# Kernel optimization log

Hardware: AMD Instinct MI355X
Metric: run time of the kernel (lower is better)

Reference implementation:

```python
import jax, jax.numpy as jnp
import numpy as np

N_NODES = 50000
N_EDGES = 800000
N_GRAPHS = 128
IN, HID, OUT, CLS = 128, 128, 128, 10


def setup_inputs() -> dict:
    key = jax.random.key(0)
    ks = jax.random.split(key, 16)
    d = {}
    d["features"] = jax.random.normal(ks[0], (N_NODES, IN), jnp.float32)
    d["edge_src"] = jax.random.randint(ks[1], (N_EDGES,), 0, N_NODES)
    d["edge_dst"] = jax.random.randint(ks[2], (N_EDGES,), 0, N_NODES)
    d["graph_ids"] = jnp.sort(jax.random.randint(ks[3], (N_NODES,), 0, N_GRAPHS))

    def lin(k, i, o):
        return (jax.random.normal(k, (i, o), jnp.float32) / np.float32(np.sqrt(i)))

    dims = [(IN, HID), (HID, HID), (HID, OUT)]
    for l, (i, o) in enumerate(dims):
        d[f"Ws{l}"] = lin(ks[4 + 3 * l], i, o)
        d[f"Wn{l}"] = lin(ks[5 + 3 * l], i, o)
        d[f"b{l}"] = jnp.zeros((o,), jnp.float32)
    d["Wf"] = lin(ks[13], OUT, CLS)
    d["bf"] = jnp.zeros((CLS,), jnp.float32)
    return d


def _sage_mean_layer(h, edge_src, edge_dst, Ws, Wn, b, in_deg):
    # mean-aggregate in-neighbor features: gather at src, segment-sum at dst
    msg_sum = jax.ops.segment_sum(h[edge_src], edge_dst, num_segments=N_NODES)
    h_neigh = msg_sum / in_deg  # [N, d], zero-degree nodes divide by 1 -> 0
    return jax.nn.relu(h @ Ws + h_neigh @ Wn + b)


def reference(features, edge_src, edge_dst, graph_ids,
              Ws0, Wn0, b0, Ws1, Wn1, b1, Ws2, Wn2, b2, Wf, bf):
    ones = jnp.ones((N_EDGES,), jnp.float32)
    in_deg = jax.ops.segment_sum(ones, edge_dst, num_segments=N_NODES)
    in_deg = jnp.maximum(in_deg, 1.0)[:, None]  # [N, 1]

    h = features
    h = _sage_mean_layer(h, edge_src, edge_dst, Ws0, Wn0, b0, in_deg)
    h = _sage_mean_layer(h, edge_src, edge_dst, Ws1, Wn1, b1, in_deg)
    h = _sage_mean_layer(h, edge_src, edge_dst, Ws2, Wn2, b2, in_deg)

    # mean graph pooling over node segments
    node_ones = jnp.ones((N_NODES,), jnp.float32)
    counts = jax.ops.segment_sum(node_ones, graph_ids, num_segments=N_GRAPHS)
    counts = jnp.maximum(counts, 1.0)[:, None]
    pooled = jax.ops.segment_sum(h, graph_ids, num_segments=N_GRAPHS) / counts

    return pooled @ Wf + bf  # [N_GRAPHS, CLS]
```

## Files before the change

kernel.cpp:

```cpp
#include <hip/hip_runtime.h>

#define N_NODES  50000
#define N_EDGES  800000
#define N_GRAPHS 128
#define HD       128
#define K2       256
#define CLS      10
#define NB_SCAN  ((N_NODES + 255) / 256)
#define NPART    8
#define PSIZE    (N_NODES / NPART)
#define NBIN     400
#define CHUNK    (N_EDGES / NBIN)
#define PCAP     131072

typedef __attribute__((ext_vector_type(8))) _Float16 f16x8;
typedef __attribute__((ext_vector_type(4))) float f32x4;
typedef __attribute__((ext_vector_type(2))) float f32x2;

union U4H8 { uint4 u; _Float16 h[8]; };
union U2H4 { uint2 u; _Float16 h[4]; };

typedef const __attribute__((address_space(1))) void* gptr_t;
typedef __attribute__((address_space(3))) void* lptr_t;
#define GLOAD_LDS16(g, l) \
    __builtin_amdgcn_global_load_lds((gptr_t)(g), (lptr_t)(l), 16, 0, 0)

__global__ __launch_bounds__(256) void k_zero(int* __restrict__ z) {
    int i = blockIdx.x * 256 + threadIdx.x;
    if (i < 50008) z[i] = 0;
}

__global__ __launch_bounds__(256) void k_initbin(
    const float* __restrict__ f, unsigned short* __restrict__ c0, unsigned char* __restrict__ f8,
    const float* __restrict__ Ws0, const float* __restrict__ Wn0,
    const float* __restrict__ Ws1, const float* __restrict__ Wn1,
    const float* __restrict__ Ws2, const float* __restrict__ Wn2,
    unsigned short* __restrict__ wt, float* __restrict__ pooled,
    const int* __restrict__ gid, float* __restrict__ counts, int* __restrict__ bflag,
    const int* __restrict__ src, const int* __restrict__ dst,
    int2* __restrict__ stag, int* __restrict__ gcount, int* __restrict__ deg) {
    if (blockIdx.x < NBIN) {
        __shared__ int lcount[NPART];
        __shared__ int lbase[NPART];
        const int tid = threadIdx.x;
        const int lane = tid & 63;
        const int lo = blockIdx.x * CHUNK;
        if (tid < NPART) lcount[tid] = 0;
        __syncthreads();
        for (int i = lo + tid; i < lo + CHUNK; i += 256) {
            int d = dst[i];
            atomicAdd(&deg[d], 1);
            int p = d / PSIZE;
#pragma unroll
            for (int q = 0; q < NPART; ++q) {
                unsigned long long m = __ballot(p == q);
                if (p == q) {
                    int leader = __ffsll((long long)m) - 1;
                    if (lane == leader) atomicAdd(&lcount[q], (int)__popcll(m));
                }
            }
        }
        __syncthreads();
        if (tid < NPART) {
            lbase[tid] = atomicAdd(&gcount[tid], lcount[tid]);
            lcount[tid] = 0;
        }
        __syncthreads();
        for (int i = lo + tid; i < lo + CHUNK; i += 256) {
            int d = dst[i];
            int p = d / PSIZE;
            int slot = 0;
#pragma unroll
            for (int q = 0; q < NPART; ++q) {
                unsigned long long m = __ballot(p == q);
                if (p == q) {
                    int leader = __ffsll((long long)m) - 1;
                    int rank = (int)__popcll(m & ((1ull << lane) - 1ull));
                    int base;
                    if (lane == leader) base = atomicAdd(&lcount[q], (int)__popcll(m));
                    base = __shfl(base, leader);
                    slot = base + rank;
                }
            }
            stag[(size_t)p * PCAP + lbase[p] + slot] = make_int2(src[i], d);
        }
        return;
    }
    long long gi = (long long)(blockIdx.x - NBIN) * 256 + threadIdx.x;
    if (gi < 800000) {
        int t = (int)gi;
        int row = t >> 4, c8 = (t & 15) * 8;
        const float* p = f + (size_t)row * HD + c8;
        float4 a = *(const float4*)p;
        float4 b = *(const float4*)(p + 4);
        U4H8 v;
        v.h[0] = (_Float16)a.x; v.h[1] = (_Float16)a.y;
        v.h[2] = (_Float16)a.z; v.h[3] = (_Float16)a.w;
        v.h[4] = (_Float16)b.x; v.h[5] = (_Float16)b.y;
        v.h[6] = (_Float16)b.z; v.h[7] = (_Float16)b.w;
        *(uint4*)(c0 + (size_t)row * K2 + c8) = v.u;
        int p0 = __builtin_amdgcn_cvt_pk_fp8_f32(a.x, a.y, 0, false);
        p0 = __builtin_amdgcn_cvt_pk_fp8_f32(a.z, a.w, p0, true);
        int p1 = __builtin_amdgcn_cvt_pk_fp8_f32(b.x, b.y, 0, false);
        p1 = __builtin_amdgcn_cvt_pk_fp8_f32(b.z, b.w, p1, true);
        *(uint2*)(f8 + (size_t)row * HD + c8) = make_uint2((unsigned)p0, (unsigned)p1);
        return;
    }
    gi -= 800000;
    if (gi < 3 * HD * K2) {
        int t = (int)gi;
        int l = t / (HD * K2), r = t % (HD * K2);
        int n = r / K2, k = r % K2;
        const float* Ws = (l == 0) ? Ws0 : (l == 1) ? Ws1 : Ws2;
        const float* Wn = (l == 0) ? Wn0 : (l == 1) ? Wn1 : Wn2;
        float w = (k < HD) ? Ws[k * HD + n] : Wn[(k - HD) * HD + n];
        union { unsigned short u; _Float16 h; } c;
        c.h = (_Float16)w;
        wt[t] = c.u;
        return;
    }
    gi -= 3 * HD * K2;
    if (gi < N_GRAPHS * HD) { pooled[gi] = 0.f; return; }
    gi -= (long long)N_GRAPHS * HD;
    if (gi < N_GRAPHS) {
        int g = (int)gi;
        int lo = 0, hi = N_NODES;
        while (lo < hi) { int mid = (lo + hi) >> 1; if (gid[mid] < g) lo = mid + 1; else hi = mid; }
        int start = lo;
        lo = 0; hi = N_NODES;
        while (lo < hi) { int mid = (lo + hi) >> 1; if (gid[mid] <= g) lo = mid + 1; else hi = mid; }
        counts[g] = (float)(lo - start);
        return;
    }
    gi -= N_GRAPHS;
    if (gi < 256) bflag[gi] = 0;
}
#define INIT_ITEMS (800000 + 3 * HD * K2 + N_GRAPHS * HD + N_GRAPHS + 256)
#define INIT_BLOCKS ((INIT_ITEMS + 255) / 256)

__global__ __launch_bounds__(256) void k_scan(const int* __restrict__ deg,
                                              int* __restrict__ rowptr, int* __restrict__ cursor,
                                              int* __restrict__ bsum, int* __restrict__ bflag) {
    __shared__ int s[256];
    __shared__ int r[256];
    const int tid = threadIdx.x;
    const int b = blockIdx.x;
    const int i = b * 256 + tid;
    int v = (i < N_NODES) ? deg[i] : 0;
    s[tid] = v;
    __syncthreads();
    for (int off = 1; off < 256; off <<= 1) {
        int add = (tid >= off) ? s[tid - off] : 0;
        __syncthreads();
        s[tid] += add;
        __syncthreads();
    }
    if (tid == 255) {
        __hip_atomic_store(&bsum[b], s[255], __ATOMIC_RELAXED, __HIP_MEMORY_SCOPE_AGENT);
        __hip_atomic_store(&bflag[b], 1, __ATOMIC_RELEASE, __HIP_MEMORY_SCOPE_AGENT);
    }
    int agg = 0;
    if (tid < b) {
        while (__hip_atomic_load(&bflag[tid], __ATOMIC_ACQUIRE, __HIP_MEMORY_SCOPE_AGENT) == 0) {}
        agg = __hip_atomic_load(&bsum[tid], __ATOMIC_RELAXED, __HIP_MEMORY_SCOPE_AGENT);
    }
    r[tid] = agg;
    __syncthreads();
    for (int off = 128; off > 0; off >>= 1) {
        if (tid < off) r[tid] += r[tid + off];
        __syncthreads();
    }
    if (i < N_NODES) {
        int val = r[0] + s[tid] - v;
        rowptr[i] = val;
        cursor[i] = val;
    }
    if (b == NB_SCAN - 1 && tid == 0) rowptr[N_NODES] = N_EDGES;
}

__global__ __launch_bounds__(256) void k_fill2(const int2* __restrict__ stag, const int* __restrict__ gcount,
                                               int* __restrict__ cursor, int* __restrict__ eidx) {
    const int part = blockIdx.x & (NPART - 1);
    const int blk = blockIdx.x >> 3;
    const int n = gcount[part];
    const int2* s = stag + (size_t)part * PCAP;
    for (int i = blk * 256 + threadIdx.x; i < n; i += 64 * 256) {
        int2 e = s[i];
        int pos = atomicAdd(&cursor[e.y], 1);
        eidx[pos] = e.x;
    }
}

__global__ __launch_bounds__(256) void k_gather(const unsigned char* __restrict__ h8,
                                                const int* __restrict__ rowptr,
                                                const int* __restrict__ eidx,
                                                unsigned short* __restrict__ msg) {
    const int node = (blockIdx.x * 256 + threadIdx.x) >> 6;
    const int lane = threadIdx.x & 63;
    if (node >= N_NODES) return;
    const int epar = lane >> 4;
    const int d0 = (lane & 15) * 8;
    const int beg = rowptr[node], end = rowptr[node + 1];
    float acc[8] = {0.f, 0.f, 0.f, 0.f, 0.f, 0.f, 0.f, 0.f};
    int j = beg + epar;
    for (; j + 12 < end; j += 16) {
        int s0 = eidx[j], s1 = eidx[j + 4], s2 = eidx[j + 8], s3 = eidx[j + 12];
        uint2 v0 = *(const uint2*)(h8 + (size_t)s0 * HD + d0);
        uint2 v1 = *(const uint2*)(h8 + (size_t)s1 * HD + d0);
        uint2 v2 = *(const uint2*)(h8 + (size_t)s2 * HD + d0);
        uint2 v3 = *(const uint2*)(h8 + (size_t)s3 * HD + d0);
        f32x2 e;
        e = __builtin_amdgcn_cvt_pk_f32_fp8(v0.x, false); acc[0] += e[0]; acc[1] += e[1];
        e = __builtin_amdgcn_cvt_pk_f32_fp8(v0.x, true);  acc[2] += e[0]; acc[3] += e[1];
        e = __builtin_amdgcn_cvt_pk_f32_fp8(v0.y, false); acc[4] += e[0]; acc[5] += e[1];
        e = __builtin_amdgcn_cvt_pk_f32_fp8(v0.y, true);  acc[6] += e[0]; acc[7] += e[1];
        e = __builtin_amdgcn_cvt_pk_f32_fp8(v1.x, false); acc[0] += e[0]; acc[1] += e[1];
        e = __builtin_amdgcn_cvt_pk_f32_fp8(v1.x, true);  acc[2] += e[0]; acc[3] += e[1];
        e = __builtin_amdgcn_cvt_pk_f32_fp8(v1.y, false); acc[4] += e[0]; acc[5] += e[1];
        e = __builtin_amdgcn_cvt_pk_f32_fp8(v1.y, true);  acc[6] += e[0]; acc[7] += e[1];
        e = __builtin_amdgcn_cvt_pk_f32_fp8(v2.x, false); acc[0] += e[0]; acc[1] += e[1];
        e = __builtin_amdgcn_cvt_pk_f32_fp8(v2.x, true);  acc[2] += e[0]; acc[3] += e[1];
        e = __builtin_amdgcn_cvt_pk_f32_fp8(v2.y, false); acc[4] += e[0]; acc[5] += e[1];
        e = __builtin_amdgcn_cvt_pk_f32_fp8(v2.y, true);  acc[6] += e[0]; acc[7] += e[1];
        e = __builtin_amdgcn_cvt_pk_f32_fp8(v3.x, false); acc[0] += e[0]; acc[1] += e[1];
        e = __builtin_amdgcn_cvt_pk_f32_fp8(v3.x, true);  acc[2] += e[0]; acc[3] += e[1];
        e = __builtin_amdgcn_cvt_pk_f32_fp8(v3.y, false); acc[4] += e[0]; acc[5] += e[1];
        e = __builtin_amdgcn_cvt_pk_f32_fp8(v3.y, true);  acc[6] += e[0]; acc[7] += e[1];
    }
    for (; j < end; j += 4) {
        uint2 v0 = *(const uint2*)(h8 + (size_t)eidx[j] * HD + d0);
        f32x2 e;
        e = __builtin_amdgcn_cvt_pk_f32_fp8(v0.x, false); acc[0] += e[0]; acc[1] += e[1];
        e = __builtin_amdgcn_cvt_pk_f32_fp8(v0.x, true);  acc[2] += e[0]; acc[3] += e[1];
        e = __builtin_amdgcn_cvt_pk_f32_fp8(v0.y, false); acc[4] += e[0]; acc[5] += e[1];
        e = __builtin_amdgcn_cvt_pk_f32_fp8(v0.y, true);  acc[6] += e[0]; acc[7] += e[1];
    }
#pragma unroll
    for (int i = 0; i < 8; ++i) {
        acc[i] += __shfl_xor(acc[i], 16);
        acc[i] += __shfl_xor(acc[i], 32);
    }
    if (epar == 0) {
        float inv = (end > beg) ? 1.0f / (float)(end - beg) : 0.f;
        U4H8 o;
#pragma unroll
        for (int i = 0; i < 8; ++i) o.h[i] = (_Float16)(acc[i] * inv);
        *(uint4*)(msg + (size_t)node * K2 + HD + d0) = o.u;
    }
}

__global__ __launch_bounds__(256) void k_sage(const unsigned short* __restrict__ hin,
                                              const unsigned short* __restrict__ wt,
                                              const float* __restrict__ bias,
                                              unsigned short* __restrict__ hout,
                                              unsigned char* __restrict__ hout8,
                                              int write16) {
    __shared__ __align__(16) _Float16 Ah[2][128 * 64];
    __shared__ __align__(16) _Float16 Bw[2][128 * 64];
    const int tid = threadIdx.x;
    const int wv = tid >> 6, lane = tid & 63;
    const int m0 = blockIdx.x * 128;
    const int m_off = (wv >> 1) * 64, n_off = (wv & 1) * 64;
    const int l15 = lane & 15, q = lane >> 4;

    f32x4 acc[4][4];
#pragma unroll
    for (int a = 0; a < 4; ++a)
#pragma unroll
        for (int b = 0; b < 4; ++b) acc[a][b] = (f32x4){0.f, 0.f, 0.f, 0.f};

    auto stage = [&](int bsel, int kt) {
        const int k0 = kt * 64;
#pragma unroll
        for (int i = 0; i < 4; ++i) {
            int idx = tid + i * 256;
            int row = idx >> 3, c = idx & 7;
            int qs = (c ^ (row & 7)) * 8;
            int gm = m0 + row;
            if (gm < N_NODES)
                GLOAD_LDS16(hin + (size_t)gm * K2 + k0 + qs, &Ah[bsel][idx * 8]);
            GLOAD_LDS16(wt + (size_t)row * K2 + k0 + qs, &Bw[bsel][idx * 8]);
        }
    };

    stage(0, 0);
    __syncthreads();
#pragma unroll
    for (int kt = 0; kt < 4; ++kt) {
        const int b = kt & 1;
        if (kt < 3) stage(b ^ 1, kt + 1);
        f16x8 hf[4][2], wf[4][2];
#pragma unroll
        for (int mt = 0; mt < 4; ++mt) {
            const int row = m_off + mt * 16 + l15;
            const int sw = row & 7;
#pragma unroll
            for (int ks = 0; ks < 2; ++ks)
                hf[mt][ks] = *(const f16x8*)&Ah[b][row * 64 + (((ks * 4 + q) ^ sw) * 8)];
        }
#pragma unroll
        for (int nt = 0; nt < 4; ++nt) {
            const int row = n_off + nt * 16 + l15;
            const int sw = row & 7;
#pragma unroll
            for (int ks = 0; ks < 2; ++ks)
                wf[nt][ks] = *(const f16x8*)&Bw[b][row * 64 + (((ks * 4 + q) ^ sw) * 8)];
        }
#pragma unroll
        for (int mt = 0; mt < 4; ++mt)
#pragma unroll
            for (int nt = 0; nt < 4; ++nt) {
                acc[mt][nt] = __builtin_amdgcn_mfma_f32_16x16x32_f16(wf[nt][0], hf[mt][0], acc[mt][nt], 0, 0, 0);
                acc[mt][nt] = __builtin_amdgcn_mfma_f32_16x16x32_f16(wf[nt][1], hf[mt][1], acc[mt][nt], 0, 0, 0);
            }
        __syncthreads();
    }
#pragma unroll
    for (int nt = 0; nt < 4; ++nt) {
        int n = n_off + nt * 16 + q * 4;
        float4 bv = *(const float4*)(bias + n);
#pragma unroll
        for (int mt = 0; mt < 4; ++mt) {
            int m = m0 + m_off + mt * 16 + l15;
            if (m < N_NODES) {
                f32x4 a = acc[mt][nt];
                float r0 = fmaxf(a[0] + bv.x, 0.f);
                float r1 = fmaxf(a[1] + bv.y, 0.f);
                float r2 = fmaxf(a[2] + bv.z, 0.f);
                float r3 = fmaxf(a[3] + bv.w, 0.f);
                if (write16) {
                    U2H4 v;
                    v.h[0] = (_Float16)r0; v.h[1] = (_Float16)r1;
                    v.h[2] = (_Float16)r2; v.h[3] = (_Float16)r3;
                    *(uint2*)(hout + (size_t)m * K2 + n) = v.u;
                }
                int p = __builtin_amdgcn_cvt_pk_fp8_f32(r0, r1, 0, false);
                p = __builtin_amdgcn_cvt_pk_fp8_f32(r2, r3, p, true);
                *(unsigned int*)(hout8 + (size_t)m * HD + n) = (unsigned)p;
            }
        }
    }
}

__global__ __launch_bounds__(256) void k_pool(const unsigned char* __restrict__ h8,
                                              const int* __restrict__ gid,
                                              float* __restrict__ pooled) {
    const int p2 = (threadIdx.x & 63) * 2;
    const int sl = threadIdx.x >> 6;
    const int n0 = blockIdx.x * 128;
    float a0 = 0.f, a1 = 0.f;
    int cur = -1;
    for (int i = sl; i < 128; i += 4) {
        int n = n0 + i;
        if (n >= N_NODES) break;
        int g = gid[n];
        if (g != cur) {
            if (cur >= 0) {
                atomicAdd(&pooled[(size_t)cur * HD + p2], a0);
                atomicAdd(&pooled[(size_t)cur * HD + p2 + 1], a1);
            }
            a0 = 0.f; a1 = 0.f;
            cur = g;
        }
        unsigned short v = *(const unsigned short*)(h8 + (size_t)n * HD + p2);
        f32x2 e = __builtin_amdgcn_cvt_pk_f32_fp8((unsigned)v, false);
        a0 += e[0]; a1 += e[1];
    }
    if (cur >= 0) {
        atomicAdd(&pooled[(size_t)cur * HD + p2], a0);
        atomicAdd(&pooled[(size_t)cur * HD + p2 + 1], a1);
    }
}

__global__ __launch_bounds__(256) void k_final(const float* __restrict__ pooled,
                                               const float* __restrict__ counts,
                                               const float* __restrict__ Wf,
                                               const float* __restrict__ bf,
                                               float* __restrict__ out) {
    int t = blockIdx.x * 256 + threadIdx.x;
    if (t >= N_GRAPHS * CLS) return;
    int g = t / CLS, c = t % CLS;
    float inv = 1.0f / fmaxf(counts[g], 1.0f);
    float s = 0.f;
    for (int k = 0; k < HD; ++k) s += pooled[(size_t)g * HD + k] * Wf[k * CLS + c];
    out[t] = s * inv + bf[c];
}

extern "C" void kernel_launch(void* const* d_in, const int* in_sizes, int n_in,
                              void* d_out, int out_size, void* d_ws, size_t ws_size,
                              hipStream_t stream) {
    const float* features = (const float*)d_in[0];
    const int*   esrc     = (const int*)d_in[1];
    const int*   edst     = (const int*)d_in[2];
    const int*   gids     = (const int*)d_in[3];
    const float* bs[3]  = {(const float*)d_in[6], (const float*)d_in[9], (const float*)d_in[12]};
    const float* Wf = (const float*)d_in[13];
    const float* bfv = (const float*)d_in[14];
    float* out = (float*)d_out;

    int* deg_i  = (int*)d_ws;
    int* gcount = deg_i + 50000;
    int* rowptr = deg_i + 50064;
    int* cursor = rowptr + 50064;
    int* bsum   = cursor + 50048;
    int* bflag  = bsum + 256;
    int* eidx   = bflag + 256;
    int2* stag  = (int2*)(eidx + 800000);
    float* pooled = (float*)(stag + (size_t)NPART * PCAP);
    float* counts = pooled + N_GRAPHS * HD;
    unsigned short* C0 = (unsigned short*)(counts + 128);
    unsigned short* C1 = C0 + (size_t)N_NODES * K2;
    unsigned short* C2 = C1 + (size_t)N_NODES * K2;
    unsigned short* Wt = C2 + (size_t)N_NODES * K2;
    unsigned char* F0 = (unsigned char*)(Wt + 3 * HD * K2);
    unsigned char* F1 = F0 + (size_t)N_NODES * HD;
    unsigned char* F2 = F1 + (size_t)N_NODES * HD;

    k_zero<<<196, 256, 0, stream>>>(deg_i);

    k_initbin<<<NBIN + INIT_BLOCKS, 256, 0, stream>>>(
        features, C0, F0,
        (const float*)d_in[4], (const float*)d_in[5],
        (const float*)d_in[7], (const float*)d_in[8],
        (const float*)d_in[10], (const float*)d_in[11],
        Wt, pooled, gids, counts, bflag,
        esrc, edst, stag, gcount, deg_i);

    k_scan<<<NB_SCAN, 256, 0, stream>>>(deg_i, rowptr, cursor, bsum, bflag);
    k_fill2<<<NPART * 64, 256, 0, stream>>>(stag, gcount, cursor, eidx);

    unsigned short* C[4] = {C0, C1, C2, C0};
    unsigned char* F[4] = {F0, F1, F2, F0};
    for (int l = 0; l < 3; ++l) {
        k_gather<<<(N_NODES * 64 + 255) / 256, 256, 0, stream>>>(F[l], rowptr, eidx, C[l]);
        k_sage<<<(N_NODES + 127) / 128, 256, 0, stream>>>(
            C[l], Wt + (size_t)l * HD * K2, bs[l], C[l + 1], F[l + 1], (l < 2) ? 1 : 0);
    }

    k_pool<<<(N_NODES + 127) / 128, 256, 0, stream>>>(F0, gids, pooled);
    k_final<<<(N_GRAPHS * CLS + 255) / 256, 256, 0, stream>>>(pooled, counts, Wf, bfv, out);
}
```

Baseline: 335.2 us.

## Pack edge staging into 32-bit words and simplify binning with more blocks

Edges staged per destination partition are now packed as one 32-bit word: 16-bit source plus 16-bit destination offset within the partition. This halves staging write and read traffic in the binning and fill kernels. The binning pass uses four times as many blocks, each holding its two edges per thread in registers instead of re-reading dst. It replaces the ballot-based aggregated shared-memory atomics with plain per-edge shared atomics. The packing depends on node ids fitting in 16 bits, which holds for 50000 nodes, and more contended LDS atomics may offset some of the gain.

```diff
diff --git a/kernel.cpp b/kernel.cpp
--- a/kernel.cpp
+++ b/kernel.cpp
@@ -9,7 +9,7 @@
 #define NB_SCAN  ((N_NODES + 255) / 256)
 #define NPART    8
 #define PSIZE    (N_NODES / NPART)
-#define NBIN     400
+#define NBIN     1600
 #define CHUNK    (N_EDGES / NBIN)
 #define PCAP     131072
 
@@ -38,26 +38,24 @@
     unsigned short* __restrict__ wt, float* __restrict__ pooled,
     const int* __restrict__ gid, float* __restrict__ counts, int* __restrict__ bflag,
     const int* __restrict__ src, const int* __restrict__ dst,
-    int2* __restrict__ stag, int* __restrict__ gcount, int* __restrict__ deg) {
+    unsigned* __restrict__ stag, int* __restrict__ gcount, int* __restrict__ deg) {
     if (blockIdx.x < NBIN) {
         __shared__ int lcount[NPART];
         __shared__ int lbase[NPART];
         const int tid = threadIdx.x;
-        const int lane = tid & 63;
         const int lo = blockIdx.x * CHUNK;
         if (tid < NPART) lcount[tid] = 0;
         __syncthreads();
-        for (int i = lo + tid; i < lo + CHUNK; i += 256) {
-            int d = dst[i];
-            atomicAdd(&deg[d], 1);
-            int p = d / PSIZE;
-#pragma unroll
-            for (int q = 0; q < NPART; ++q) {
-                unsigned long long m = __ballot(p == q);
-                if (p == q) {
-                    int leader = __ffsll((long long)m) - 1;
-                    if (lane == leader) atomicAdd(&lcount[q], (int)__popcll(m));
-                }
+        int dc[2], sc[2];
+#pragma unroll
+        for (int it = 0; it < 2; ++it) {
+            int i = lo + tid + it * 256;
+            dc[it] = -1;
+            if (i < lo + CHUNK) {
+                int d = dst[i];
+                dc[it] = d; sc[it] = src[i];
+                atomicAdd(&deg[d], 1);
+                atomicAdd(&lcount[d / PSIZE], 1);
             }
         }
         __syncthreads();
@@ -66,23 +64,14 @@
             lcount[tid] = 0;
         }
         __syncthreads();
-        for (int i = lo + tid; i < lo + CHUNK; i += 256) {
-            int d = dst[i];
-            int p = d / PSIZE;
-            int slot = 0;
-#pragma unroll
-            for (int q = 0; q < NPART; ++q) {
-                unsigned long long m = __ballot(p == q);
-                if (p == q) {
-                    int leader = __ffsll((long long)m) - 1;
-                    int rank = (int)__popcll(m & ((1ull << lane) - 1ull));
-                    int base;
-                    if (lane == leader) base = atomicAdd(&lcount[q], (int)__popcll(m));
-                    base = __shfl(base, leader);
-                    slot = base + rank;
-                }
+#pragma unroll
+        for (int it = 0; it < 2; ++it) {
+            if (dc[it] >= 0) {
+                int p = dc[it] / PSIZE;
+                int slot = atomicAdd(&lcount[p], 1);
+                stag[(size_t)p * PCAP + lbase[p] + slot] =
+                    (unsigned)sc[it] | ((unsigned)(dc[it] - p * PSIZE) << 16);
             }
-            stag[(size_t)p * PCAP + lbase[p] + slot] = make_int2(src[i], d);
         }
         return;
     }
@@ -178,16 +167,18 @@
     if (b == NB_SCAN - 1 && tid == 0) rowptr[N_NODES] = N_EDGES;
 }
 
-__global__ __launch_bounds__(256) void k_fill2(const int2* __restrict__ stag, const int* __restrict__ gcount,
+__global__ __launch_bounds__(256) void k_fill2(const unsigned* __restrict__ stag, const int* __restrict__ gcount,
                                                int* __restrict__ cursor, int* __restrict__ eidx) {
     const int part = blockIdx.x & (NPART - 1);
     const int blk = blockIdx.x >> 3;
     const int n = gcount[part];
-    const int2* s = stag + (size_t)part * PCAP;
+    const unsigned* s = stag + (size_t)part * PCAP;
     for (int i = blk * 256 + threadIdx.x; i < n; i += 64 * 256) {
-        int2 e = s[i];
-        int pos = atomicAdd(&cursor[e.y], 1);
-        eidx[pos] = e.x;
+        unsigned v = s[i];
+        int srcv = (int)(v & 0xFFFFu);
+        int dstv = part * PSIZE + (int)(v >> 16);
+        int pos = atomicAdd(&cursor[dstv], 1);
+        eidx[pos] = srcv;
     }
 }
 
@@ -405,7 +396,7 @@
     int* bsum   = cursor + 50048;
     int* bflag  = bsum + 256;
     int* eidx   = bflag + 256;
-    int2* stag  = (int2*)(eidx + 800000);
+    unsigned* stag = (unsigned*)(eidx + 800000);
     float* pooled = (float*)(stag + (size_t)NPART * PCAP);
     float* counts = pooled + N_GRAPHS * HD;
     unsigned short* C0 = (unsigned short*)(counts + 128);
```

Measured after the change: 339.4 us. About the same (+1.3%).
